# Performance work log

Measured on AMD Instinct MI355X. Metric: run time of the kernel, lower is better.

## Reference

```python
import jax, jax.numpy as jnp
import numpy as np


def setup_inputs() -> dict:
    key = jax.random.key(0)
    ks = jax.random.split(key, 6)
    B, V, T, Fin = 16, 12288, 4, 64
    Kv, Kt, Fout = 4, 4, 64
    NNZ = 9 * V  # ~8 neighbors + self loop per vertex (HEALPix)
    inputs = jax.random.normal(ks[0], (B, V, T, Fin), dtype=jnp.float32)
    std = np.sqrt(2.0 / (Fin * Kv * Kt))
    weight = jax.random.normal(ks[1], (Fin, Kv, Kt, Fout), dtype=jnp.float32) * std
    bias = jnp.zeros((Fout,), dtype=jnp.float32)
    lap_rows = jax.random.randint(ks[2], (NNZ,), 0, V, dtype=jnp.int32)
    lap_cols = jax.random.randint(ks[3], (NNZ,), 0, V, dtype=jnp.int32)
    # small values so the Chebyshev recurrence stays numerically tame
    lap_vals = jax.random.normal(ks[4], (NNZ,), dtype=jnp.float32) * 0.1
    return {"inputs": inputs, "weight": weight, "bias": bias,
            "lap_vals": lap_vals, "lap_rows": lap_rows, "lap_cols": lap_cols}


def _cheb_conv_temp(inputs, weight, lap_vals, lap_rows, lap_cols):
    B, V, T, Fin = inputs.shape
    Fin_w, Kv, Kt, Fout = weight.shape
    # x0: [V, T*Fin*B] matching torch permute(1,2,3,0).view
    x0 = jnp.transpose(inputs, (1, 2, 3, 0)).reshape(V, T * Fin * B)

    def spmm(x):  # sparse laplacian @ x via gather + segment_sum
        return jax.ops.segment_sum(lap_vals[:, None] * x[lap_cols], lap_rows,
                                   num_segments=V)

    xs = [x0]
    if Kv > 1:
        x1 = spmm(x0)
        xs.append(x1)
        for _ in range(2, Kv):
            x2 = 2.0 * spmm(x1) - x0
            xs.append(x2)
            x0, x1 = x1, x2
    x = jnp.stack(xs, axis=0).reshape(Kv, V, T, Fin, B)
    # contraction aligns flattened (Fin,Kv,T) of x with (Fin,Kv,Kt) of weight
    return jnp.einsum('kvtfb,fkto->bvo', x, weight)


def reference(inputs, weight, bias, lap_vals, lap_rows, lap_cols):
    out = _cheb_conv_temp(inputs, weight, lap_vals, lap_rows, lap_cols)
    return out + bias
```

## Files before the change

### kernel.cpp

```cpp
#include <hip/hip_runtime.h>

#define V_N 12288
#define B_N 16
#define TF_N 256
#define ROW2 1024
#define FOUT 64

typedef __attribute__((ext_vector_type(8))) short short8;
typedef __attribute__((ext_vector_type(4))) float f32x4;

__device__ __forceinline__ unsigned short f2bf(float x){
  unsigned u = __float_as_uint(x);
  return (unsigned short)((u + 0x7FFFu + ((u >> 16) & 1u)) >> 16);
}
__device__ __forceinline__ float bf2f(unsigned short h){
  return __uint_as_float(((unsigned)h) << 16);
}

__global__ void k_zero(int* __restrict__ p, int n){
  int i = blockIdx.x * 256 + threadIdx.x;
  if (i < n) p[i] = 0;
}

__global__ void k_hist(const int* __restrict__ rows, int* __restrict__ cnt, int nnz){
  int i = blockIdx.x * 256 + threadIdx.x;
  if (i < nnz) atomicAdd(&cnt[rows[i]], 1);
}

__global__ void k_scan(const int* __restrict__ cnt, int* __restrict__ rp){
  __shared__ int part[256];
  __shared__ int base[257];
  int t = threadIdx.x;
  const int per = V_N / 256;
  int s = 0;
  for (int i = 0; i < per; ++i) s += cnt[t * per + i];
  part[t] = s;
  __syncthreads();
  if (t == 0){
    int run = 0;
    for (int i = 0; i < 256; ++i){ base[i] = run; run += part[i]; }
    base[256] = run;
  }
  __syncthreads();
  int run = base[t];
  for (int i = 0; i < per; ++i){ rp[t * per + i] = run; run += cnt[t * per + i]; }
  if (t == 255) rp[V_N] = run;
}

__global__ void k_scatter(const int* __restrict__ rows, const int* __restrict__ cols,
                          const float* __restrict__ vals, const int* __restrict__ rp,
                          int* __restrict__ cur, int* __restrict__ cols_s,
                          float* __restrict__ vals_s, int nnz){
  int i = blockIdx.x * 256 + threadIdx.x;
  if (i < nnz){
    int r = rows[i];
    int pos = rp[r] + atomicAdd(&cur[r], 1);
    cols_s[pos] = cols[i];
    vals_s[pos] = vals[i];
  }
}

__global__ void k_convw(const float* __restrict__ w, unsigned short* __restrict__ wb){
  int i = blockIdx.x * 256 + threadIdx.x;
  int j = i & 7;
  int l = (i >> 3) & 63;
  int n = (i >> 9) & 3;
  int s = (i >> 11) & 7;
  int k = (i >> 14) & 3;
  int kk = s * 32 + ((l >> 4) << 3) + j;
  int t = kk >> 6, f = kk & 63;
  int o = (n << 4) + (l & 15);
  wb[i] = f2bf(w[((f * 4 + k) * 4 + t) * 64 + o]);
}

__global__ __launch_bounds__(256, 4) void k_proj(
                       const float* __restrict__ in, const unsigned short* __restrict__ wb,
                       unsigned short* __restrict__ y0, unsigned short* __restrict__ y1,
                       unsigned short* __restrict__ y2, unsigned short* __restrict__ y3){
  __shared__ unsigned short As[32 * 256];
  char* lds = (char*)As;
  int t = threadIdx.x;
  int vb = blockIdx.x >> 4;
  int b  = blockIdx.x & 15;
  int v0 = vb * 32;
  const float* src = in + ((size_t)b * V_N + v0) * TF_N;
  #pragma unroll
  for (int i = 0; i < 8; ++i){
    int flat = i * 1024 + t * 4;
    int r  = flat >> 8;
    int c2 = (flat & 255) * 2;
    float4 f = *(const float4*)(src + flat);
    unsigned long long pk =  (unsigned long long)f2bf(f.x)
                          | ((unsigned long long)f2bf(f.y) << 16)
                          | ((unsigned long long)f2bf(f.z) << 32)
                          | ((unsigned long long)f2bf(f.w) << 48);
    *(unsigned long long*)(lds + ((r * 512 + c2) ^ ((r & 7) << 4))) = pk;
  }
  __syncthreads();

  int lane = t & 63;
  int k    = t >> 6;
  int colL = lane & 15, rg = lane >> 4;
  f32x4 acc[2][4];
  #pragma unroll
  for (int mt = 0; mt < 2; ++mt)
    #pragma unroll
    for (int n = 0; n < 4; ++n) acc[mt][n] = (f32x4){0.f, 0.f, 0.f, 0.f};

  const unsigned short* wk = wb + k * 16384;
  #pragma unroll
  for (int s = 0; s < 8; ++s){
    int c2 = rg * 16 + s * 64;
    short8 a0 = *(const short8*)(lds + (( colL       * 512 + c2) ^ ((colL & 7) << 4)));
    short8 a1 = *(const short8*)(lds + (((16 + colL) * 512 + c2) ^ ((colL & 7) << 4)));
    #pragma unroll
    for (int n = 0; n < 4; ++n){
      short8 bf = *(const short8*)(wk + ((s * 4 + n) << 9) + lane * 8);
      acc[0][n] = __builtin_amdgcn_mfma_f32_16x16x32_bf16(a0, bf, acc[0][n], 0, 0, 0);
      acc[1][n] = __builtin_amdgcn_mfma_f32_16x16x32_bf16(a1, bf, acc[1][n], 0, 0, 0);
    }
  }
  unsigned short* yk = (k == 0) ? y0 : (k == 1) ? y1 : (k == 2) ? y2 : y3;
  #pragma unroll
  for (int mt = 0; mt < 2; ++mt)
    #pragma unroll
    for (int n = 0; n < 4; ++n)
      #pragma unroll
      for (int r = 0; r < 4; ++r)
        yk[(size_t)(v0 + mt * 16 + rg * 4 + r) * ROW2 + b * 64 + n * 16 + colL]
            = f2bf(acc[mt][n][r]);
}

__global__ void k_spmm2(const unsigned short* __restrict__ src,
                        const unsigned short* __restrict__ addA,
                        const unsigned short* __restrict__ subB,
                        unsigned short* __restrict__ dst,
                        const int* __restrict__ rp, const int* __restrict__ cols,
                        const float* __restrict__ vals, float alpha){
  int lane = threadIdx.x & 63;
  int r = blockIdx.x * 4 + (threadIdx.x >> 6);
  int j0 = lane * 16;
  float acc[16];
  #pragma unroll
  for (int p = 0; p < 16; ++p) acc[p] = 0.f;
  int beg = rp[r], end = rp[r + 1];
  for (int i = beg; i < end; ++i){
    float val = vals[i];
    int c = cols[i];
    const unsigned short* srow = src + (size_t)c * ROW2 + j0;
    short8 a0 = *(const short8*)srow;
    short8 a1 = *(const short8*)(srow + 8);
    #pragma unroll
    for (int p = 0; p < 8; ++p) acc[p]     += val * bf2f((unsigned short)a0[p]);
    #pragma unroll
    for (int p = 0; p < 8; ++p) acc[p + 8] += val * bf2f((unsigned short)a1[p]);
  }
  const unsigned short* arow = addA + (size_t)r * ROW2 + j0;
  short8 q0 = *(const short8*)arow;
  short8 q1 = *(const short8*)(arow + 8);
  #pragma unroll
  for (int p = 0; p < 8; ++p) acc[p]     = alpha * acc[p]     + bf2f((unsigned short)q0[p]);
  #pragma unroll
  for (int p = 0; p < 8; ++p) acc[p + 8] = alpha * acc[p + 8] + bf2f((unsigned short)q1[p]);
  if (subB){
    const unsigned short* brow = subB + (size_t)r * ROW2 + j0;
    short8 s0 = *(const short8*)brow;
    short8 s1 = *(const short8*)(brow + 8);
    #pragma unroll
    for (int p = 0; p < 8; ++p) acc[p]     -= bf2f((unsigned short)s0[p]);
    #pragma unroll
    for (int p = 0; p < 8; ++p) acc[p + 8] -= bf2f((unsigned short)s1[p]);
  }
  unsigned short* drow = dst + (size_t)r * ROW2 + j0;
  short8 o0, o1;
  #pragma unroll
  for (int p = 0; p < 8; ++p) o0[p] = (short)f2bf(acc[p]);
  #pragma unroll
  for (int p = 0; p < 8; ++p) o1[p] = (short)f2bf(acc[p + 8]);
  *(short8*)drow = o0;
  *(short8*)(drow + 8) = o1;
}

__global__ void k_final(const unsigned short* __restrict__ src,
                        const unsigned short* __restrict__ y0,
                        const unsigned short* __restrict__ b2,
                        const float* __restrict__ bias,
                        float* __restrict__ out,
                        const int* __restrict__ rp, const int* __restrict__ cols,
                        const float* __restrict__ vals){
  int lane = threadIdx.x & 63;
  int v = blockIdx.x * 4 + (threadIdx.x >> 6);
  int j0 = lane * 16;
  float acc[16];
  #pragma unroll
  for (int p = 0; p < 16; ++p) acc[p] = 0.f;
  int beg = rp[v], end = rp[v + 1];
  for (int i = beg; i < end; ++i){
    float val = vals[i];
    int c = cols[i];
    const unsigned short* srow = src + (size_t)c * ROW2 + j0;
    short8 a0 = *(const short8*)srow;
    short8 a1 = *(const short8*)(srow + 8);
    #pragma unroll
    for (int p = 0; p < 8; ++p) acc[p]     += val * bf2f((unsigned short)a0[p]);
    #pragma unroll
    for (int p = 0; p < 8; ++p) acc[p + 8] += val * bf2f((unsigned short)a1[p]);
  }
  const unsigned short* yrow = y0 + (size_t)v * ROW2 + j0;
  const unsigned short* brow = b2 + (size_t)v * ROW2 + j0;
  short8 q0 = *(const short8*)yrow;
  short8 q1 = *(const short8*)(yrow + 8);
  short8 s0 = *(const short8*)brow;
  short8 s1 = *(const short8*)(brow + 8);
  #pragma unroll
  for (int p = 0; p < 8; ++p) acc[p]     += bf2f((unsigned short)q0[p]) - bf2f((unsigned short)s0[p]);
  #pragma unroll
  for (int p = 0; p < 8; ++p) acc[p + 8] += bf2f((unsigned short)q1[p]) - bf2f((unsigned short)s1[p]);
  int b = lane >> 2;
  int o0 = (lane & 3) * 16;
  float* obase = out + ((size_t)b * V_N + v) * FOUT + o0;
  #pragma unroll
  for (int p = 0; p < 16; ++p) obase[p] = acc[p] + bias[o0 + p];
}

extern "C" void kernel_launch(void* const* d_in, const int* in_sizes, int n_in,
                              void* d_out, int out_size, void* d_ws, size_t ws_size,
                              hipStream_t stream) {
  const float* inputs   = (const float*)d_in[0];
  const float* weight   = (const float*)d_in[1];
  const float* bias     = (const float*)d_in[2];
  const float* lap_vals = (const float*)d_in[3];
  const int*   lap_rows = (const int*)d_in[4];
  const int*   lap_cols = (const int*)d_in[5];
  float* out = (float*)d_out;
  int nnz = in_sizes[3];

  char* ws = (char*)d_ws;
  size_t off = 0;
  auto alloc = [&](size_t bytes) -> void* {
    void* p = ws + off;
    off += (bytes + 255) & ~(size_t)255;
    return p;
  };
  const size_t YB = (size_t)V_N * ROW2 * 2;
  unsigned short* y0 = (unsigned short*)alloc(YB);
  unsigned short* y1 = (unsigned short*)alloc(YB);
  unsigned short* y2 = (unsigned short*)alloc(YB);
  unsigned short* y3 = (unsigned short*)alloc(YB);
  unsigned short* c2 = (unsigned short*)alloc(YB);
  unsigned short* c1 = (unsigned short*)alloc(YB);
  unsigned short* wb = (unsigned short*)alloc(65536 * 2);
  int*   cnt   = (int*)alloc(V_N * 4);
  int*   cur   = (int*)alloc(V_N * 4);
  int*   rp    = (int*)alloc((V_N + 1) * 4);
  int*   colss = (int*)alloc((size_t)nnz * 4);
  float* valss = (float*)alloc((size_t)nnz * 4);

  k_zero<<<(2 * V_N + 255) / 256, 256, 0, stream>>>(cnt, 2 * V_N);
  k_hist<<<(nnz + 255) / 256, 256, 0, stream>>>(lap_rows, cnt, nnz);
  k_scan<<<1, 256, 0, stream>>>(cnt, rp);
  k_scatter<<<(nnz + 255) / 256, 256, 0, stream>>>(lap_rows, lap_cols, lap_vals, rp, cur,
                                                   colss, valss, nnz);
  k_convw<<<65536 / 256, 256, 0, stream>>>(weight, wb);
  k_proj<<<(V_N / 32) * B_N, 256, 0, stream>>>(inputs, wb, y0, y1, y2, y3);

  k_spmm2<<<V_N / 4, 256, 0, stream>>>(y3, y2, nullptr, c2, rp, colss, valss, 2.0f);
  k_spmm2<<<V_N / 4, 256, 0, stream>>>(c2, y1, y3, c1, rp, colss, valss, 2.0f);
  k_final<<<V_N / 4, 256, 0, stream>>>(c1, y0, c2, bias, out, rp, colss, valss);
}
```

Measured before the change: 245.5 us.

## Permute projection output columns for vectorized stores and prefetch operands in k_proj

In k_proj, all eight float4 input loads are issued before bf16 conversion, and the weight and LDS A-operand loads are double-buffered one step ahead of the MFMAs. The output columns are permuted within each 64-wide chunk so every thread writes four packed bf16 values as one 8-byte store instead of scalar 2-byte stores. The final kernel is changed to undo this permutation, so it writes float4 output plus bias instead of sixteen scalar stores. Occupancy hint drops from 4 to 3 blocks to leave room for the extra registers, which may reduce latency hiding.

```diff
diff --git a/kernel.cpp b/kernel.cpp
--- a/kernel.cpp
+++ b/kernel.cpp
@@ -73,7 +73,7 @@
   wb[i] = f2bf(w[((f * 4 + k) * 4 + t) * 64 + o]);
 }
 
-__global__ __launch_bounds__(256, 4) void k_proj(
+__global__ __launch_bounds__(256, 3) void k_proj(
                        const float* __restrict__ in, const unsigned short* __restrict__ wb,
                        unsigned short* __restrict__ y0, unsigned short* __restrict__ y1,
                        unsigned short* __restrict__ y2, unsigned short* __restrict__ y3){
@@ -84,16 +84,18 @@
   int b  = blockIdx.x & 15;
   int v0 = vb * 32;
   const float* src = in + ((size_t)b * V_N + v0) * TF_N;
+  float4 f[8];
+  #pragma unroll
+  for (int i = 0; i < 8; ++i) f[i] = *(const float4*)(src + i * 1024 + t * 4);
   #pragma unroll
   for (int i = 0; i < 8; ++i){
     int flat = i * 1024 + t * 4;
     int r  = flat >> 8;
     int c2 = (flat & 255) * 2;
-    float4 f = *(const float4*)(src + flat);
-    unsigned long long pk =  (unsigned long long)f2bf(f.x)
-                          | ((unsigned long long)f2bf(f.y) << 16)
-                          | ((unsigned long long)f2bf(f.z) << 32)
-                          | ((unsigned long long)f2bf(f.w) << 48);
+    unsigned long long pk =  (unsigned long long)f2bf(f[i].x)
+                          | ((unsigned long long)f2bf(f[i].y) << 16)
+                          | ((unsigned long long)f2bf(f[i].z) << 32)
+                          | ((unsigned long long)f2bf(f[i].w) << 48);
     *(unsigned long long*)(lds + ((r * 512 + c2) ^ ((r & 7) << 4))) = pk;
   }
   __syncthreads();
@@ -107,28 +109,45 @@
     #pragma unroll
     for (int n = 0; n < 4; ++n) acc[mt][n] = (f32x4){0.f, 0.f, 0.f, 0.f};
 
-  const unsigned short* wk = wb + k * 16384;
+  const unsigned short* wk = wb + k * 16384 + lane * 8;
+  const char* aL0 = lds + (size_t)0;
+  short8 wbuf[2][4];
+  short8 abuf[2][2];
+  #pragma unroll
+  for (int n = 0; n < 4; ++n) wbuf[0][n] = *(const short8*)(wk + (n << 9));
+  {
+    int c2 = rg * 16;
+    abuf[0][0] = *(const short8*)(lds + (( colL       * 512 + c2) ^ ((colL & 7) << 4)));
+    abuf[0][1] = *(const short8*)(lds + (((16 + colL) * 512 + c2) ^ ((colL & 7) << 4)));
+  }
   #pragma unroll
   for (int s = 0; s < 8; ++s){
-    int c2 = rg * 16 + s * 64;
-    short8 a0 = *(const short8*)(lds + (( colL       * 512 + c2) ^ ((colL & 7) << 4)));
-    short8 a1 = *(const short8*)(lds + (((16 + colL) * 512 + c2) ^ ((colL & 7) << 4)));
+    int cur = s & 1, nxt = cur ^ 1;
+    if (s < 7){
+      #pragma unroll
+      for (int n = 0; n < 4; ++n)
+        wbuf[nxt][n] = *(const short8*)(wk + (((s + 1) * 4 + n) << 9));
+      int c2 = rg * 16 + (s + 1) * 64;
+      abuf[nxt][0] = *(const short8*)(lds + (( colL       * 512 + c2) ^ ((colL & 7) << 4)));
+      abuf[nxt][1] = *(const short8*)(lds + (((16 + colL) * 512 + c2) ^ ((colL & 7) << 4)));
+    }
     #pragma unroll
     for (int n = 0; n < 4; ++n){
-      short8 bf = *(const short8*)(wk + ((s * 4 + n) << 9) + lane * 8);
-      acc[0][n] = __builtin_amdgcn_mfma_f32_16x16x32_bf16(a0, bf, acc[0][n], 0, 0, 0);
-      acc[1][n] = __builtin_amdgcn_mfma_f32_16x16x32_bf16(a1, bf, acc[1][n], 0, 0, 0);
+      acc[0][n] = __builtin_amdgcn_mfma_f32_16x16x32_bf16(abuf[cur][0], wbuf[cur][n], acc[0][n], 0, 0, 0);
+      acc[1][n] = __builtin_amdgcn_mfma_f32_16x16x32_bf16(abuf[cur][1], wbuf[cur][n], acc[1][n], 0, 0, 0);
     }
   }
   unsigned short* yk = (k == 0) ? y0 : (k == 1) ? y1 : (k == 2) ? y2 : y3;
   #pragma unroll
   for (int mt = 0; mt < 2; ++mt)
     #pragma unroll
-    for (int n = 0; n < 4; ++n)
-      #pragma unroll
-      for (int r = 0; r < 4; ++r)
-        yk[(size_t)(v0 + mt * 16 + rg * 4 + r) * ROW2 + b * 64 + n * 16 + colL]
-            = f2bf(acc[mt][n][r]);
+    for (int r = 0; r < 4; ++r){
+      int v = v0 + mt * 16 + rg * 4 + r;
+      unsigned lo = (unsigned)f2bf(acc[mt][0][r]) | ((unsigned)f2bf(acc[mt][1][r]) << 16);
+      unsigned hi = (unsigned)f2bf(acc[mt][2][r]) | ((unsigned)f2bf(acc[mt][3][r]) << 16);
+      uint2 pk = {lo, hi};
+      *(uint2*)(yk + (size_t)v * ROW2 + b * 64 + colL * 4) = pk;
+    }
 }
 
 __global__ void k_spmm2(const unsigned short* __restrict__ src,
@@ -217,10 +236,18 @@
   #pragma unroll
   for (int p = 0; p < 8; ++p) acc[p + 8] += bf2f((unsigned short)q1[p]) - bf2f((unsigned short)s1[p]);
   int b = lane >> 2;
-  int o0 = (lane & 3) * 16;
-  float* obase = out + ((size_t)b * V_N + v) * FOUT + o0;
-  #pragma unroll
-  for (int p = 0; p < 16; ++p) obase[p] = acc[p] + bias[o0 + p];
+  int c0 = (lane & 3) * 4;
+  float* obase = out + ((size_t)b * V_N + v) * FOUT;
+  #pragma unroll
+  for (int n = 0; n < 4; ++n){
+    float4 bv = *(const float4*)(bias + n * 16 + c0);
+    float4 w;
+    w.x = acc[0 * 4 + n] + bv.x;
+    w.y = acc[1 * 4 + n] + bv.y;
+    w.z = acc[2 * 4 + n] + bv.z;
+    w.w = acc[3 * 4 + n] + bv.w;
+    *(float4*)(obase + n * 16 + c0) = w;
+  }
 }
 
 extern "C" void kernel_launch(void* const* d_in, const int* in_sizes, int n_in,
```

Result: faster. 234.9 us (-4.3%).
